# Kernel optimization log

Measured on AMD Instinct MI355X. Metric: run time of the kernel, lower is better.

## Reference

```python
import jax, jax.numpy as jnp
import numpy as np

H = 64          # hidden_size
NG = 5000       # num_genes
B = 32          # num_graphs
N = B * NG      # total nodes
E = 1_600_000   # total edges


def setup_inputs() -> dict:
    key = jax.random.key(0)
    ks = jax.random.split(key, 32)
    def nrm(k, shape, s=0.05):
        return jax.random.normal(k, shape, jnp.float32) * s
    return {
        "x": jax.random.normal(ks[0], (N, 2), jnp.float32),
        "edge_index": jax.random.randint(ks[1], (2, E), 0, N),
        # pert_w: Linear(1, H); gene_basal_w: Linear(1, H)
        "pert_w_W": nrm(ks[2], (H, 1)), "pert_w_b": nrm(ks[3], (H,)),
        "basal_W": nrm(ks[4], (H, 1)), "basal_b": nrm(ks[5], (H,)),
        # gene embedding table (max_norm=True -> rows renormed to norm<=1)
        "emb_table": nrm(ks[6], (NG, H), 0.5),
        # emb_trans: Linear(2H, H)
        "emb_trans_W": nrm(ks[7], (H, 2 * H)), "emb_trans_b": nrm(ks[8], (H,)),
        # pert_base_trans_w: Linear(2H, H)  (gene_pert_agg == 'concat+w')
        "pbt_W": nrm(ks[9], (H, 2 * H)), "pbt_b": nrm(ks[10], (H,)),
        # two GCNConv(H, H) layers
        "gcn1_W": nrm(ks[11], (H, H)), "gcn1_b": nrm(ks[12], (H,)),
        "gcn2_W": nrm(ks[13], (H, H)), "gcn2_b": nrm(ks[14], (H,)),
        # recovery_w: MLP([H, 2H, H, 1]) with BN on first two hidden layers
        "rec_W1": nrm(ks[15], (2 * H, H)), "rec_b1": nrm(ks[16], (2 * H,)),
        "rec_g1": jnp.ones((2 * H,), jnp.float32), "rec_be1": jnp.zeros((2 * H,), jnp.float32),
        "rec_W2": nrm(ks[17], (H, 2 * H)), "rec_b2": nrm(ks[18], (H,)),
        "rec_g2": jnp.ones((H,), jnp.float32), "rec_be2": jnp.zeros((H,), jnp.float32),
        "rec_W3": nrm(ks[19], (1, H)), "rec_b3": nrm(ks[20], (1,)),
    }


def _gcn_conv(h, src, dst, norm, W, b, n_nodes):
    # PyG GCNConv: x' = scatter_add(norm * (x W^T)[src] -> dst) + b, self-loops included in src/dst
    m = h @ W.T                                   # [N, H]
    out = jax.ops.segment_sum(m[src] * norm[:, None], dst, num_segments=n_nodes)
    return out + b


def _batchnorm(z, g, b, eps=1e-5):
    mu = z.mean(0)
    var = z.var(0)
    return (z - mu) * jax.lax.rsqrt(var + eps) * g + b


def reference(x, edge_index, pert_w_W, pert_w_b, basal_W, basal_b, emb_table,
              emb_trans_W, emb_trans_b, pbt_W, pbt_b, gcn1_W, gcn1_b,
              gcn2_W, gcn2_b, rec_W1, rec_b1, rec_g1, rec_be1,
              rec_W2, rec_b2, rec_g2, rec_be2, rec_W3, rec_b3):
    n_nodes = x.shape[0]
    ng = emb_table.shape[0]
    nb = n_nodes // ng

    # GCN normalization with self-loops (computed once, shared by both layers)
    loop = jnp.arange(n_nodes)
    src = jnp.concatenate([edge_index[0], loop])
    dst = jnp.concatenate([edge_index[1], loop])
    deg = jax.ops.segment_sum(jnp.ones_like(src, jnp.float32), dst, num_segments=n_nodes)
    dinv = jnp.where(deg > 0, jax.lax.rsqrt(jnp.maximum(deg, 1.0)), 0.0)
    norm = dinv[src] * dinv[dst]

    pert_emb = x[:, 1:2] @ pert_w_W.T + pert_w_b          # [N, H]
    base = x[:, 0:1] @ basal_W.T + basal_b                # [N, H]

    # nn.Embedding(max_norm=True): renorm rows to max L2 norm of 1
    nrm = jnp.linalg.norm(emb_table, axis=1, keepdims=True)
    emb_n = emb_table * jnp.minimum(1.0, 1.0 / jnp.maximum(nrm, 1e-7))
    emb = jnp.tile(emb_n, (nb, 1))                        # arange(NG).repeat(B) lookup
    base_emb = jnp.concatenate([emb, base], axis=1) @ emb_trans_W.T + emb_trans_b

    def pbt(p, b_):
        return jnp.concatenate([p, b_], axis=1) @ pbt_W.T + pbt_b

    h = pbt(pert_emb, base_emb)
    h = pbt(jax.nn.relu(_gcn_conv(h, src, dst, norm, gcn1_W, gcn1_b, n_nodes)), base_emb)
    h = pbt(jax.nn.relu(_gcn_conv(h, src, dst, norm, gcn2_W, gcn2_b, n_nodes)), base_emb)

    # recovery_w: Linear -> BN -> ReLU -> Linear -> BN -> ReLU -> Linear
    z = jax.nn.relu(_batchnorm(h @ rec_W1.T + rec_b1, rec_g1, rec_be1))
    z = jax.nn.relu(_batchnorm(z @ rec_W2.T + rec_b2, rec_g2, rec_be2))
    out = z @ rec_W3.T + rec_b3                           # [N, 1]
    return out.reshape(nb, ng)
```

## Files before the change

kernel.cpp:

```cpp
#include <hip/hip_runtime.h>


#define GS_GRID 2048
#define GS_BLK  256

enum { A1_=0, A0_=64, C1_=128, C0_=192, D1_=256, D0_=320,
       S1_=384, Q1_=512, SC1_=640, SH1_=768,
       S2_=896, Q2_=960, SC2_=1024, SH2_=1088,
       GD1_=1152, GA1_=1216, G00_=1280,
       GD2_=1344, G02_=1408, RD1_=1472, RD0_=1600, CST_FLOATS=2048 };

__device__ __forceinline__ float wave_sum64(float v) {
#pragma unroll
  for (int o = 32; o; o >>= 1) v += __shfl_xor(v, o, 64);
  return v;
}

__device__ __forceinline__ int rfl(int v) { return __builtin_amdgcn_readfirstlane(v); }

__device__ __forceinline__ float rlane(float v, int k) {
  return __int_as_float(__builtin_amdgcn_readlane(__float_as_int(v), k));
}


__global__ __launch_bounds__(256) void hist_k(const int* __restrict__ ei,
                                              int* __restrict__ hist, int E) {
  __shared__ int h[256];
  const int t = threadIdx.x;
  h[t] = 0;
  __syncthreads();
  const int per = (E + gridDim.x - 1) / gridDim.x;
  const int beg = blockIdx.x * per, end = min(E, beg + per);
  for (int i = beg + t; i < end; i += 256)
    atomicAdd(&h[ei[E + i] >> 10], 1);
  __syncthreads();
  hist[blockIdx.x * 256 + t] = h[t];
}

__global__ void scan1b_k(int* __restrict__ hist, int* __restrict__ bsum) {
  __shared__ int sc[256];
  const int t = threadIdx.x;
  const int b = blockIdx.x;
  int v = hist[t * 256 + b];
  sc[t] = v; __syncthreads();
  for (int o = 1; o < 256; o <<= 1) {
    int x = sc[t]; if (t >= o) x += sc[t - o];
    __syncthreads(); sc[t] = x; __syncthreads();
  }
  hist[t * 256 + b] = sc[t] - v;
  if (t == 255) bsum[b] = sc[t];
}

__global__ void scan2b_k(const int* __restrict__ bsum, int* __restrict__ bucketBase,
                         int* __restrict__ rowptrN, int E) {
  __shared__ int sc[256];
  const int t = threadIdx.x;
  int v = bsum[t];
  sc[t] = v; __syncthreads();
  for (int o = 1; o < 256; o <<= 1) {
    int x = sc[t]; if (t >= o) x += sc[t - o];
    __syncthreads(); sc[t] = x; __syncthreads();
  }
  bucketBase[t] = sc[t] - v;
  if (t == 255) { bucketBase[256] = sc[t]; rowptrN[0] = E; }
}

__global__ __launch_bounds__(256) void bucket_k(const int* __restrict__ ei,
                                                const int* __restrict__ hist,
                                                const int* __restrict__ bucketBase,
                                                int2* __restrict__ eb, int E) {
  __shared__ int cur[256];
  const int t = threadIdx.x;
  cur[t] = hist[blockIdx.x * 256 + t] + bucketBase[t];
  __syncthreads();
  const int per = (E + gridDim.x - 1) / gridDim.x;
  const int beg = blockIdx.x * per, end = min(E, beg + per);
// ... 69 lines not shown
  }
  cst[A1_ + h] = a1; cst[A0_ + h] = a0; cst[C1_ + h] = c1; cst[C0_ + h] = c0 + etB[h];
}

__global__ void consts2_k(const float* __restrict__ pbtW, const float* __restrict__ pbtB,
                          float* __restrict__ cst) {
  int h = threadIdx.x;
  float d1 = 0, d0 = 0;
  for (int k = 0; k < 64; ++k) {
    float w = pbtW[h * 128 + 64 + k];
    d1 = fmaf(w, cst[C1_ + k], d1);
    d0 = fmaf(w, cst[C0_ + k], d0);
  }
  cst[D1_ + h] = d1; cst[D0_ + h] = d0 + pbtB[h];
}

__global__ void consts3_k(const float* __restrict__ g1W, float* __restrict__ cst) {
  int h = threadIdx.x;
  float gd1 = 0, ga1 = 0, g00 = 0;
  for (int k = 0; k < 64; ++k) {
    float w = g1W[h * 64 + k];
    gd1 = fmaf(w, cst[D1_ + k], gd1);
    ga1 = fmaf(w, cst[A1_ + k], ga1);
    g00 = fmaf(w, cst[D0_ + k] + cst[A0_ + k], g00);
  }
  cst[GD1_ + h] = gd1; cst[GA1_ + h] = ga1; cst[G00_ + h] = g00;
}

__global__ void consts5_k(const float* __restrict__ g2W, float* __restrict__ cst) {
  int h = threadIdx.x;
  float a = 0, b = 0;
  for (int k = 0; k < 64; ++k) {
    float w = g2W[h * 64 + k];
    a = fmaf(w, cst[D1_ + k], a);
    b = fmaf(w, cst[D0_ + k], b);
  }
  cst[GD2_ + h] = a; cst[G02_ + h] = b;
}

__global__ void consts6_k(const float* __restrict__ rW1, const float* __restrict__ rb1,
                          float* __restrict__ cst) {
  int c = threadIdx.x;
  float a = 0, b = 0;
  for (int k = 0; k < 64; ++k) {
    float w = rW1[c * 64 + k];
    a = fmaf(w, cst[D1_ + k], a);
    b = fmaf(w, cst[D0_ + k], b);
  }
  cst[RD1_ + c] = a; cst[RD0_ + c] = b + rb1[c];
}

__global__ void constsW_k(const float* __restrict__ g2W, const float* __restrict__ rW1,
                          const float* __restrict__ pbtW,
                          float* __restrict__ Wf, float* __restrict__ Wr) {
  const int t = threadIdx.x;
  for (int e = t; e < 4096; e += 256) {
    int c = e >> 6, j = e & 63;
    float s = 0.f;
    for (int h = 0; h < 64; ++h) s = fmaf(g2W[c * 64 + h], pbtW[h * 128 + j], s);
    Wf[e] = s;
  }
  for (int e = t; e < 8192; e += 256) {
    int c = e >> 6, j = e & 63;
    float s = 0.f;
    for (int h = 0; h < 64; ++h) s = fmaf(rW1[c * 64 + h], pbtW[h * 128 + j], s);
    Wr[e] = s;
  }
}

template <bool NORM>
__global__ __launch_bounds__(256) void geneT_k(const float* __restrict__ in,
                                               const float* __restrict__ W, int ldw,
                                               float* __restrict__ out, int NG) {
  const int lane = threadIdx.x & 63;
  const int wid = blockIdx.x * 4 + (threadIdx.x >> 6);
  const int nw = gridDim.x * 4;
  float w[64];
#pragma unroll
  for (int j = 0; j < 16; ++j) {
    float4 v = *reinterpret_cast<const float4*>(W + lane * ldw + 4 * j);
    w[4 * j] = v.x; w[4 * j + 1] = v.y; w[4 * j + 2] = v.z; w[4 * j + 3] = v.w;
  }
  for (int g = wid; g < NG; g += nw) {
    float e = in[g * 64 + lane];
    if (NORM) {
      float sq = wave_sum64(e * e);
      float nrm = sqrtf(sq);
      float s = nrm > 1.f ? 1.f / nrm : 1.f;
      e *= s;
    }
    float acc = 0.f;
#pragma unroll
    for (int k = 0; k < 64; ++k) acc = fmaf(w[k], rlane(e, k), acc);
    out[g * 64 + lane] = acc;
  }
}

__global__ __launch_bounds__(256) void m1_k(const float* __restrict__ x,
                                            const float* __restrict__ embTm1,
                                            const float* __restrict__ dinv,
                                            const float* __restrict__ cst,
                                            float* __restrict__ m1, int N, int NG) {
  int total = N * 16;
  for (int idx = blockIdx.x * blockDim.x + threadIdx.x; idx < total;
       idx += gridDim.x * blockDim.x) {
    int n = idx >> 4, q = idx & 15;
    int g = n % NG;
    float x0 = x[2 * n], x1 = x[2 * n + 1], dn = dinv[n];
    float4 em = *reinterpret_cast<const float4*>(embTm1 + g * 64 + q * 4);
    float4 gd1 = *reinterpret_cast<const float4*>(cst + GD1_ + q * 4);
    float4 ga1 = *reinterpret_cast<const float4*>(cst + GA1_ + q * 4);
    float4 g00 = *reinterpret_cast<const float4*>(cst + G00_ + q * 4);
    float4 mv;
    mv.x = dn * (fmaf(x0, gd1.x, fmaf(x1, ga1.x, em.x + g00.x)));
    mv.y = dn * (fmaf(x0, gd1.y, fmaf(x1, ga1.y, em.y + g00.y)));
    mv.z = dn * (fmaf(x0, gd1.z, fmaf(x1, ga1.z, em.z + g00.z)));
    mv.w = dn * (fmaf(x0, gd1.w, fmaf(x1, ga1.w, em.w + g00.w)));
    reinterpret_cast<float4*>(m1)[idx] = mv;
  }
}

#define XS_STRIDE 130
#define WS_STRIDE 68
#define OS_STRIDE 68
#define OS_WORDS  (128 * OS_STRIDE)
#define WS_WORDS  (64 * WS_STRIDE)
#define LDS_WORDS (OS_WORDS + WS_WORDS + 128)

template <bool MUL_D>
__global__ __launch_bounds__(256, 4) void gemmt_gv_k(
    const float* __restrict__ in,
    const float* __restrict__ W,
    const float* __restrict__ tbl,
    const float* __restrict__ cA,
    const float* __restrict__ cB,
    const float* __restrict__ x,
    const float* __restrict__ dinv,
    float* __restrict__ out, int ldout, int N, int NG) {
  __shared__ float lds[LDS_WORDS];
  float* Xs = lds;
  float* Ws = lds + OS_WORDS;
  const int t = threadIdx.x;
  const int base = blockIdx.x << 7;

#pragma unroll
  for (int c = 0; c < 16; ++c) {
    int lin = c * 256 + t;
    int cw = lin >> 6, kw = lin & 63;
    Ws[kw * WS_STRIDE + cw] = W[cw * 64 + kw];
  }
#pragma unroll
  for (int c = 0; c < 8; ++c) {
    int lin = c * 256 + t;
    int nl = lin >> 4, k4 = lin & 15;
    int row = base + nl; if (row >= N) row = N - 1;
    float4 v = *reinterpret_cast<const float4*>(in + (size_t)row * 64 + 4 * k4);
    Xs[(4 * k4 + 0) * XS_STRIDE + nl] = v.x;
    Xs[(4 * k4 + 1) * XS_STRIDE + nl] = v.y;
    Xs[(4 * k4 + 2) * XS_STRIDE + nl] = v.z;
    Xs[(4 * k4 + 3) * XS_STRIDE + nl] = v.w;
  }
  __syncthreads();

  const int ng = t & 31;
  const int c0 = (t >> 5) * 8;
  float acc[8][4];
#pragma unroll
  for (int i = 0; i < 8; ++i)
#pragma unroll
    for (int j = 0; j < 4; ++j) acc[i][j] = 0.f;
#pragma unroll 4
  for (int k = 0; k < 64; ++k) {
    float4 wa = *reinterpret_cast<const float4*>(Ws + k * WS_STRIDE + c0);
    float4 wb = *reinterpret_cast<const float4*>(Ws + k * WS_STRIDE + c0 + 4);
    float2 xa = *reinterpret_cast<const float2*>(Xs + k * XS_STRIDE + 2 * ng);
    float2 xb = *reinterpret_cast<const float2*>(Xs + k * XS_STRIDE + 2 * ng + 64);
    const float w8[8] = {wa.x, wa.y, wa.z, wa.w, wb.x, wb.y, wb.z, wb.w};
    const float x4[4] = {xa.x, xa.y, xb.x, xb.y};
#pragma unroll
    for (int ci = 0; ci < 8; ++ci)
#pragma unroll
      for (int xi = 0; xi < 4; ++xi)
        acc[ci][xi] = fmaf(w8[ci], x4[xi], acc[ci][xi]);
  }
  __syncthreads();

  const int nd[4] = {2 * ng, 2 * ng + 1, 2 * ng + 64, 2 * ng + 65};
#pragma unroll
  for (int ci = 0; ci < 8; ++ci) {
    Xs[nd[0] * OS_STRIDE + c0 + ci] = acc[ci][0];
    Xs[nd[1] * OS_STRIDE + c0 + ci] = acc[ci][1];
    Xs[nd[2] * OS_STRIDE + c0 + ci] = acc[ci][2];
    Xs[nd[3] * OS_STRIDE + c0 + ci] = acc[ci][3];
  }
  __syncthreads();

  const int q = t & 15;
  const float4 a4 = *reinterpret_cast<const float4*>(cA + 4 * q);
  const float4 b4 = *reinterpret_cast<const float4*>(cB + 4 * q);
#pragma unroll
  for (int c = 0; c < 8; ++c) {
    int nl = c * 16 + (t >> 4);
    int n = base + nl;
    if (n < N) {
      float4 o = *reinterpret_cast<const float4*>(Xs + nl * OS_STRIDE + 4 * q);
      int g = n % NG;
      float4 tg = *reinterpret_cast<const float4*>(tbl + (size_t)g * 64 + 4 * q);
      float x0 = x[2 * n];
      o.x += fmaf(x0, a4.x, tg.x + b4.x);
      o.y += fmaf(x0, a4.y, tg.y + b4.y);
      o.z += fmaf(x0, a4.z, tg.z + b4.z);
      o.w += fmaf(x0, a4.w, tg.w + b4.w);
      if (MUL_D) {
        float dv = dinv[n];
        o.x *= dv; o.y *= dv; o.z *= dv; o.w *= dv;
      }
      *reinterpret_cast<float4*>(out + (size_t)n * ldout + 4 * q) = o;
    }
  }
}

__global__ __launch_bounds__(256, 4) void gemmt_rec1_k(
    const float* __restrict__ in,
    const float* __restrict__ Wr,
    const float* __restrict__ tblA, const float* __restrict__ tblB,
    const float* __restrict__ cA,
    const float* __restrict__ cB,
    const float* __restrict__ x,
    float* __restrict__ Z,
    float* __restrict__ sums, float* __restrict__ sqs,
    int N, int NG) {
  __shared__ float lds[LDS_WORDS];
  float* Xs = lds;
  float* Ws = lds + OS_WORDS;
  float* sred = lds + OS_WORDS + WS_WORDS;
  const int t = threadIdx.x;
  const int base = blockIdx.x << 7;
  if (t < 128) sred[t] = 0.f;

#pragma unroll
  for (int c = 0; c < 16; ++c) {
    int lin = c * 256 + t;
    int cw = lin >> 6, kw = lin & 63;
    Ws[kw * WS_STRIDE + cw] = Wr[cw * 64 + kw];
  }
#pragma unroll
  for (int c = 0; c < 8; ++c) {
    int lin = c * 256 + t;
    int nl = lin >> 4, k4 = lin & 15;
    int row = base + nl; if (row >= N) row = N - 1;
    float4 v = *reinterpret_cast<const float4*>(in + (size_t)row * 64 + 4 * k4);
    Xs[(4 * k4 + 0) * XS_STRIDE + nl] = v.x;
    Xs[(4 * k4 + 1) * XS_STRIDE + nl] = v.y;
    Xs[(4 * k4 + 2) * XS_STRIDE + nl] = v.z;
    Xs[(4 * k4 + 3) * XS_STRIDE + nl] = v.w;
  }
  __syncthreads();

  const int ng = t & 31;
  const int c0 = (t >> 5) * 8;
  float accA[8][4], accB[8][4];
#pragma unroll
  for (int i = 0; i < 8; ++i)
#pragma unroll
    for (int j = 0; j < 4; ++j) { accA[i][j] = 0.f; accB[i][j] = 0.f; }

#pragma unroll 4
  for (int k = 0; k < 64; ++k) {
    float4 wa = *reinterpret_cast<const float4*>(Ws + k * WS_STRIDE + c0);
    float4 wb = *reinterpret_cast<const float4*>(Ws + k * WS_STRIDE + c0 + 4);
    float2 xa = *reinterpret_cast<const float2*>(Xs + k * XS_STRIDE + 2 * ng);
    float2 xb = *reinterpret_cast<const float2*>(Xs + k * XS_STRIDE + 2 * ng + 64);
    const float w8[8] = {wa.x, wa.y, wa.z, wa.w, wb.x, wb.y, wb.z, wb.w};
    const float x4[4] = {xa.x, xa.y, xb.x, xb.y};
#pragma unroll
    for (int ci = 0; ci < 8; ++ci)
#pragma unroll
      for (int xi = 0; xi < 4; ++xi)
        accA[ci][xi] = fmaf(w8[ci], x4[xi], accA[ci][xi]);
  }
  __syncthreads();
#pragma unroll
  for (int c = 0; c < 16; ++c) {
    int lin = c * 256 + t;
    int cw = lin >> 6, kw = lin & 63;
    Ws[kw * WS_STRIDE + cw] = Wr[(64 + cw) * 64 + kw];
  }
  __syncthreads();
#pragma unroll 4
  for (int k = 0; k < 64; ++k) {
    float4 wa = *reinterpret_cast<const float4*>(Ws + k * WS_STRIDE + c0);
    float4 wb = *reinterpret_cast<const float4*>(Ws + k * WS_STRIDE + c0 + 4);
    float2 xa = *reinterpret_cast<const float2*>(Xs + k * XS_STRIDE + 2 * ng);
    float2 xb = *reinterpret_cast<const float2*>(Xs + k * XS_STRIDE + 2 * ng + 64);
    const float w8[8] = {wa.x, wa.y, wa.z, wa.w, wb.x, wb.y, wb.z, wb.w};
    const float x4[4] = {xa.x, xa.y, xb.x, xb.y};
#pragma unroll
    for (int ci = 0; ci < 8; ++ci)
#pragma unroll
      for (int xi = 0; xi < 4; ++xi)
        accB[ci][xi] = fmaf(w8[ci], x4[xi], accB[ci][xi]);
  }
  __syncthreads();

  const int nd[4] = {2 * ng, 2 * ng + 1, 2 * ng + 64, 2 * ng + 65};
  const int q = t & 15;

#pragma unroll
  for (int ci = 0; ci < 8; ++ci) {
    Xs[nd[0] * OS_STRIDE + c0 + ci] = accA[ci][0];
    Xs[nd[1] * OS_STRIDE + c0 + ci] = accA[ci][1];
    Xs[nd[2] * OS_STRIDE + c0 + ci] = accA[ci][2];
    Xs[nd[3] * OS_STRIDE + c0 + ci] = accA[ci][3];
  }
  __syncthreads();
  {
    const float4 a4 = *reinterpret_cast<const float4*>(cA + 4 * q);
    const float4 b4 = *reinterpret_cast<const float4*>(cB + 4 * q);
    float4 s4 = make_float4(0.f, 0.f, 0.f, 0.f);
    float4 q4 = make_float4(0.f, 0.f, 0.f, 0.f);
#pragma unroll
    for (int c = 0; c < 8; ++c) {
      int nl = c * 16 + (t >> 4);
      int n = base + nl;
      if (n < N) {
        float4 o = *reinterpret_cast<const float4*>(Xs + nl * OS_STRIDE + 4 * q);
        int g = n % NG;
        float4 tg = *reinterpret_cast<const float4*>(tblA + (size_t)g * 64 + 4 * q);
        float x0 = x[2 * n];
        o.x += fmaf(x0, a4.x, tg.x + b4.x);
        o.y += fmaf(x0, a4.y, tg.y + b4.y);
        o.z += fmaf(x0, a4.z, tg.z + b4.z);
        o.w += fmaf(x0, a4.w, tg.w + b4.w);
        *reinterpret_cast<float4*>(Z + (size_t)n * 128 + 4 * q) = o;
        s4.x += o.x; s4.y += o.y; s4.z += o.z; s4.w += o.w;
        q4.x += o.x * o.x; q4.y += o.y * o.y; q4.z += o.z * o.z; q4.w += o.w * o.w;
      }
    }
    atomicAdd(&sred[4 * q + 0], s4.x); atomicAdd(&sred[4 * q + 1], s4.y);
    atomicAdd(&sred[4 * q + 2], s4.z); atomicAdd(&sred[4 * q + 3], s4.w);
    atomicAdd(&sred[64 + 4 * q + 0], q4.x); atomicAdd(&sred[64 + 4 * q + 1], q4.y);
    atomicAdd(&sred[64 + 4 * q + 2], q4.z); atomicAdd(&sred[64 + 4 * q + 3], q4.w);
  }
  __syncthreads();
  if (t < 64) {
    atomicAdd(&sums[t], sred[t]);
    atomicAdd(&sqs[t], sred[64 + t]);
  }
  __syncthreads();
  if (t < 128) sred[t] = 0.f;
  __syncthreads();

#pragma unroll
  for (int ci = 0; ci < 8; ++ci) {
    Xs[nd[0] * OS_STRIDE + c0 + ci] = accB[ci][0];
    Xs[nd[1] * OS_STRIDE + c0 + ci] = accB[ci][1];
    Xs[nd[2] * OS_STRIDE + c0 + ci] = accB[ci][2];
    Xs[nd[3] * OS_STRIDE + c0 + ci] = accB[ci][3];
  }
  __syncthreads();
  {
    const float4 a4 = *reinterpret_cast<const float4*>(cA + 64 + 4 * q);
    const float4 b4 = *reinterpret_cast<const float4*>(cB + 64 + 4 * q);
    float4 s4 = make_float4(0.f, 0.f, 0.f, 0.f);
    float4 q4 = make_float4(0.f, 0.f, 0.f, 0.f);
#pragma unroll
    for (int c = 0; c < 8; ++c) {
      int nl = c * 16 + (t >> 4);
      int n = base + nl;
      if (n < N) {
        float4 o = *reinterpret_cast<const float4*>(Xs + nl * OS_STRIDE + 4 * q);
        int g = n % NG;
        float4 tg = *reinterpret_cast<const float4*>(tblB + (size_t)g * 64 + 4 * q);
        float x0 = x[2 * n];
        o.x += fmaf(x0, a4.x, tg.x + b4.x);
        o.y += fmaf(x0, a4.y, tg.y + b4.y);
        o.z += fmaf(x0, a4.z, tg.z + b4.z);
        o.w += fmaf(x0, a4.w, tg.w + b4.w);
        *reinterpret_cast<float4*>(Z + (size_t)n * 128 + 64 + 4 * q) = o;
        s4.x += o.x; s4.y += o.y; s4.z += o.z; s4.w += o.w;
        q4.x += o.x * o.x; q4.y += o.y * o.y; q4.z += o.z * o.z; q4.w += o.w * o.w;
      }
    }
    atomicAdd(&sred[4 * q + 0], s4.x); atomicAdd(&sred[4 * q + 1], s4.y);
    atomicAdd(&sred[4 * q + 2], s4.z); atomicAdd(&sred[4 * q + 3], s4.w);
    atomicAdd(&sred[64 + 4 * q + 0], q4.x); atomicAdd(&sred[64 + 4 * q + 1], q4.y);
    atomicAdd(&sred[64 + 4 * q + 2], q4.z); atomicAdd(&sred[64 + 4 * q + 3], q4.w);
  }
  __syncthreads();
  if (t < 64) {
    atomicAdd(&sums[64 + t], sred[t]);
    atomicAdd(&sqs[64 + t], sred[64 + t]);
  }
}

__global__ __launch_bounds__(256, 4) void gemmt_rec2_k(
    const float* __restrict__ Z,
    const float* __restrict__ W,
    const float* __restrict__ b,
    const float* __restrict__ bnsc, const float* __restrict__ bnsh,
    float* __restrict__ out,
    float* __restrict__ sums, float* __restrict__ sqs, int N) {
  __shared__ float lds[LDS_WORDS];
  float* Xs = lds;
  float* Ws = lds + OS_WORDS;
  float* sred = lds + OS_WORDS + WS_WORDS;
  const int t = threadIdx.x;
  const int base = blockIdx.x << 7;
  if (t < 128) sred[t] = 0.f;

  const int ng = t & 31;
  const int c0 = (t >> 5) * 8;
  float acc[8][4];
#pragma unroll
  for (int i = 0; i < 8; ++i)
#pragma unroll
    for (int j = 0; j < 4; ++j) acc[i][j] = 0.f;

  for (int half = 0; half < 2; ++half) {
    if (half) __syncthreads();
    const int ko = half * 64;
#pragma unroll
    for (int c = 0; c < 16; ++c) {
      int lin = c * 256 + t;
      int cw = lin >> 6, kw = lin & 63;
      Ws[kw * WS_STRIDE + cw] = W[cw * 128 + ko + kw];
    }
#pragma unroll
    for (int c = 0; c < 8; ++c) {
      int lin = c * 256 + t;
      int nl = lin >> 4, k4 = lin & 15;
      int row = base + nl; if (row >= N) row = N - 1;
      float4 v = *reinterpret_cast<const float4*>(Z + (size_t)row * 128 + ko + 4 * k4);
      float4 sc = *reinterpret_cast<const float4*>(bnsc + ko + 4 * k4);
      float4 sh = *reinterpret_cast<const float4*>(bnsh + ko + 4 * k4);
      v.x = fmaxf(fmaf(v.x, sc.x, sh.x), 0.f);
      v.y = fmaxf(fmaf(v.y, sc.y, sh.y), 0.f);
      v.z = fmaxf(fmaf(v.z, sc.z, sh.z), 0.f);
      v.w = fmaxf(fmaf(v.w, sc.w, sh.w), 0.f);
      Xs[(4 * k4 + 0) * XS_STRIDE + nl] = v.x;
      Xs[(4 * k4 + 1) * XS_STRIDE + nl] = v.y;
      Xs[(4 * k4 + 2) * XS_STRIDE + nl] = v.z;
      Xs[(4 * k4 + 3) * XS_STRIDE + nl] = v.w;
    }
    __syncthreads();
#pragma unroll 4
    for (int k = 0; k < 64; ++k) {
      float4 wa = *reinterpret_cast<const float4*>(Ws + k * WS_STRIDE + c0);
      float4 wb = *reinterpret_cast<const float4*>(Ws + k * WS_STRIDE + c0 + 4);
      float2 xa = *reinterpret_cast<const float2*>(Xs + k * XS_STRIDE + 2 * ng);
      float2 xb = *reinterpret_cast<const float2*>(Xs + k * XS_STRIDE + 2 * ng + 64);
      const float w8[8] = {wa.x, wa.y, wa.z, wa.w, wb.x, wb.y, wb.z, wb.w};
      const float x4[4] = {xa.x, xa.y, xb.x, xb.y};
#pragma unroll
      for (int ci = 0; ci < 8; ++ci)
#pragma unroll
        for (int xi = 0; xi < 4; ++xi)
          acc[ci][xi] = fmaf(w8[ci], x4[xi], acc[ci][xi]);
    }
  }
  __syncthreads();

  const int nd[4] = {2 * ng, 2 * ng + 1, 2 * ng + 64, 2 * ng + 65};
#pragma unroll
  for (int ci = 0; ci < 8; ++ci) {
    Xs[nd[0] * OS_STRIDE + c0 + ci] = acc[ci][0];
    Xs[nd[1] * OS_STRIDE + c0 + ci] = acc[ci][1];
    Xs[nd[2] * OS_STRIDE + c0 + ci] = acc[ci][2];
    Xs[nd[3] * OS_STRIDE + c0 + ci] = acc[ci][3];
  }
  __syncthreads();

  const int q = t & 15;
  const float4 bb = *reinterpret_cast<const float4*>(b + 4 * q);
  float4 s4 = make_float4(0.f, 0.f, 0.f, 0.f);
  float4 q4 = make_float4(0.f, 0.f, 0.f, 0.f);
#pragma unroll
  for (int c = 0; c < 8; ++c) {
    int nl = c * 16 + (t >> 4);
    int n = base + nl;
    if (n < N) {
      float4 o = *reinterpret_cast<const float4*>(Xs + nl * OS_STRIDE + 4 * q);
      o.x += bb.x; o.y += bb.y; o.z += bb.z; o.w += bb.w;
      *reinterpret_cast<float4*>(out + (size_t)n * 64 + 4 * q) = o;
      s4.x += o.x; s4.y += o.y; s4.z += o.z; s4.w += o.w;
      q4.x += o.x * o.x; q4.y += o.y * o.y; q4.z += o.z * o.z; q4.w += o.w * o.w;
    }
  }
  atomicAdd(&sred[4 * q + 0], s4.x); atomicAdd(&sred[4 * q + 1], s4.y);
  atomicAdd(&sred[4 * q + 2], s4.z); atomicAdd(&sred[4 * q + 3], s4.w);
  atomicAdd(&sred[64 + 4 * q + 0], q4.x); atomicAdd(&sred[64 + 4 * q + 1], q4.y);
  atomicAdd(&sred[64 + 4 * q + 2], q4.z); atomicAdd(&sred[64 + 4 * q + 3], q4.w);
  __syncthreads();
  if (t < 64) {
    atomicAdd(&sums[t], sred[t]);
    atomicAdd(&sqs[t], sred[64 + t]);
  }
}

__global__ __launch_bounds__(256) void gather_k(const float* __restrict__ m,
                                                const int* __restrict__ rowptr,
                                                const int* __restrict__ col,
                                                const float* __restrict__ dinv,
                                                const float* __restrict__ bias,
                                                float* __restrict__ out, int N) {
  const int lane = threadIdx.x & 63;
  const int wid = blockIdx.x * 4 + (threadIdx.x >> 6);
  const int nw = gridDim.x * 4;
  const float b = bias[lane];
  for (int n = wid; n < N; n += nw) {
    const int nn = rfl(n);
    const float dn = dinv[nn];
    float a0 = m[(size_t)nn * 64 + lane];
    float a1 = 0.f, a2 = 0.f, a3 = 0.f;
    const int beg = rfl(rowptr[nn]), end = rfl(rowptr[nn + 1]);
    for (int base = beg; base < end; base += 64) {
      const int rem = end - base;
      const int kk = rem < 64 ? rem : 64;
      int cv = (lane < kk) ? col[base + lane] : 0;
      int k = 0;
      for (; k + 7 < kk; k += 8) {
        int i0 = __shfl(cv, k, 64),     i1 = __shfl(cv, k + 1, 64);
        int i2 = __shfl(cv, k + 2, 64), i3 = __shfl(cv, k + 3, 64);
        int i4 = __shfl(cv, k + 4, 64), i5 = __shfl(cv, k + 5, 64);
        int i6 = __shfl(cv, k + 6, 64), i7 = __shfl(cv, k + 7, 64);
        float v0 = m[(size_t)i0 * 64 + lane];
        float v1 = m[(size_t)i1 * 64 + lane];
        float v2 = m[(size_t)i2 * 64 + lane];
        float v3 = m[(size_t)i3 * 64 + lane];
        float v4 = m[(size_t)i4 * 64 + lane];
        float v5 = m[(size_t)i5 * 64 + lane];
        float v6 = m[(size_t)i6 * 64 + lane];
        float v7 = m[(size_t)i7 * 64 + lane];
        a0 += v0 + v4; a1 += v1 + v5; a2 += v2 + v6; a3 += v3 + v7;
      }
// ... 36 lines not shown
  const float sc = scale[lane], sh = shift[lane], w = W3[lane], b = b3[0];
  for (int n = wid; n < N; n += nw) {
    float v = z2[(size_t)n * 64 + lane];
    v = fmaxf(fmaf(v, sc, sh), 0.f) * w;
    v = wave_sum64(v);
    if (lane == 0) out[n] = v + b;
  }
}

extern "C" void kernel_launch(void* const* d_in, const int* in_sizes, int n_in,
                              void* d_out, int out_size, void* d_ws, size_t ws_size,
                              hipStream_t stream) {
  const float* x     = (const float*)d_in[0];
  const int*   ei    = (const int*)d_in[1];
  const float* pertW = (const float*)d_in[2];
  const float* pertB = (const float*)d_in[3];
  const float* basW  = (const float*)d_in[4];
  const float* basB  = (const float*)d_in[5];
  const float* embTb = (const float*)d_in[6];
  const float* etW   = (const float*)d_in[7];
  const float* etB   = (const float*)d_in[8];
  const float* pbtW  = (const float*)d_in[9];
  const float* pbtB  = (const float*)d_in[10];
  const float* g1W   = (const float*)d_in[11];
  const float* g1B   = (const float*)d_in[12];
  const float* g2W   = (const float*)d_in[13];
  const float* g2B   = (const float*)d_in[14];
  const float* rW1   = (const float*)d_in[15];
  const float* rb1   = (const float*)d_in[16];
  const float* rg1   = (const float*)d_in[17];
  const float* rbe1  = (const float*)d_in[18];
  const float* rW2   = (const float*)d_in[19];
  const float* rb2   = (const float*)d_in[20];
  const float* rg2   = (const float*)d_in[21];
  const float* rbe2  = (const float*)d_in[22];
  const float* rW3   = (const float*)d_in[23];
  const float* rb3   = (const float*)d_in[24];
  float* outp = (float*)d_out;

  const int N  = in_sizes[0] / 2;
  const int E  = in_sizes[1] / 2;
  const int NG = in_sizes[6] / 64;
  const int NB = (N + 1023) >> 10;
  const int NT = (N + 127) >> 7;

  char* p = (char*)d_ws;
  float* cst    = (float*)p; p += CST_FLOATS * 4;
  int*   hist   = (int*)p;   p += 256 * 256 * 4;
  int*   bb     = (int*)p;   p += 1024;
  int*   bsum   = (int*)p;   p += 1024;
  int*   rowptr = (int*)p;   p += (size_t)(N + 64) * 4;
  float* dinv   = (float*)p; p += (size_t)N * 4;
  int*   col    = (int*)p;   p += (size_t)E * 4;
  float* Wf     = (float*)p; p += 4096 * 4;
  float* Wr     = (float*)p; p += 8192 * 4;
  float* embT   = (float*)p; p += (size_t)NG * 64 * 4;
  float* embT2  = (float*)p; p += (size_t)NG * 64 * 4;
  float* embT2g2= (float*)p; p += (size_t)NG * 64 * 4;
  float* embT2rA= (float*)p; p += (size_t)NG * 64 * 4;
  float* embT2rB= (float*)p; p += (size_t)NG * 64 * 4;
  float* z2buf  = (float*)p; p += (size_t)N * 64 * 4;
  float* hb     = (float*)p; p += (size_t)N * 64 * 4;
  float* tmp1   = (float*)p; p += (size_t)N * 64 * 4;
  float* tmp2   = (float*)p; p += (size_t)N * 64 * 4;
  float* Z = hb;
  float* z2 = z2buf;
  float* embTm1 = embT;
  int2*  eb = (int2*)tmp2;

  dim3 blk(GS_BLK), grid(GS_GRID);

  hipMemsetAsync(cst, 0, CST_FLOATS * 4, stream);

  hist_k<<<256, 256, 0, stream>>>(ei, hist, E);
  scan1b_k<<<256, 256, 0, stream>>>(hist, bsum);
  scan2b_k<<<1, 256, 0, stream>>>(bsum, bb, rowptr + N, E);
  bucket_k<<<256, 256, 0, stream>>>(ei, hist, bb, eb, E);
  csr_k<<<NB, 256, 0, stream>>>(eb, bb, rowptr, dinv, col, N);

  consts1_k<<<1, 64, 0, stream>>>(pbtW, pertW, pertB, etW, basW, basB, etB, cst);
  consts2_k<<<1, 64, 0, stream>>>(pbtW, pbtB, cst);
  consts3_k<<<1, 64, 0, stream>>>(g1W, cst);
  consts5_k<<<1, 64, 0, stream>>>(g2W, cst);
  consts6_k<<<1, 128, 0, stream>>>(rW1, rb1, cst);
  constsW_k<<<1, 256, 0, stream>>>(g2W, rW1, pbtW, Wf, Wr);
  geneT_k<true><<<256, 256, 0, stream>>>(embTb, etW, 128, embT, NG);
  geneT_k<false><<<256, 256, 0, stream>>>(embT, pbtW + 64, 128, embT2, NG);
  geneT_k<false><<<256, 256, 0, stream>>>(embT2, g1W, 64, embTm1, NG);
  geneT_k<false><<<256, 256, 0, stream>>>(embT2, g2W, 64, embT2g2, NG);
  geneT_k<false><<<256, 256, 0, stream>>>(embT2, rW1, 64, embT2rA, NG);
  geneT_k<false><<<256, 256, 0, stream>>>(embT2, rW1 + 64 * 64, 64, embT2rB, NG);
  m1_k<<<grid, blk, 0, stream>>>(x, embTm1, dinv, cst, tmp1, N, NG);

  gather_k<<<grid, blk, 0, stream>>>(tmp1, rowptr, col, dinv, g1B, tmp2, N);
  gemmt_gv_k<true><<<NT, blk, 0, stream>>>(
      tmp2, Wf, embT2g2, cst + GD2_, cst + G02_, x, dinv, tmp1, 64, N, NG);
  gather_k<<<grid, blk, 0, stream>>>(tmp1, rowptr, col, dinv, g2B, tmp2, N);

  gemmt_rec1_k<<<NT, blk, 0, stream>>>(
      tmp2, Wr, embT2rA, embT2rB, cst + RD1_, cst + RD0_, x, Z,
      cst + S1_, cst + Q1_, N, NG);
  bnparam_k<<<1, 128, 0, stream>>>(cst + S1_, cst + Q1_, rg1, rbe1,
                                   cst + SC1_, cst + SH1_, 128, 1.0f / (float)N);
  gemmt_rec2_k<<<NT, blk, 0, stream>>>(Z, rW2, rb2, cst + SC1_, cst + SH1_,
                                       z2, cst + S2_, cst + Q2_, N);
  bnparam_k<<<1, 64, 0, stream>>>(cst + S2_, cst + Q2_, rg2, rbe2,
                                  cst + SC2_, cst + SH2_, 64, 1.0f / (float)N);
  rec3_k<<<grid, blk, 0, stream>>>(z2, cst + SC2_, cst + SH2_, rW3, rb3, outp, N);
}
```

Baseline: 485.9 us.

## Read pre-transposed GEMM weights wave-uniformly from global instead of LDS staging

The three node-wise GEMM kernels stop staging weight tiles in shared memory. They read pre-transposed weights (built once by constsW_k and a new w2t_k) directly from global memory with wave-uniform addresses, so each wave owns a slice of output columns. Thread mapping changes to 2 nodes by 16 or 32 columns per lane, and rec1 now computes all 128 outputs in one pass instead of two. This removes LDS weight traffic and some barriers, at the cost of more accumulator registers and more global/scalar weight loads per k step.

```diff
diff --git a/kernel.cpp b/kernel.cpp
--- a/kernel.cpp
+++ b/kernel.cpp
@@ -21,7 +21,6 @@
 __device__ __forceinline__ float rlane(float v, int k) {
   return __int_as_float(__builtin_amdgcn_readlane(__float_as_int(v), k));
 }
-
 
 __global__ __launch_bounds__(256) void hist_k(const int* __restrict__ ei,
                                               int* __restrict__ hist, int E) {
@@ -197,19 +196,26 @@
 
 __global__ void constsW_k(const float* __restrict__ g2W, const float* __restrict__ rW1,
                           const float* __restrict__ pbtW,
-                          float* __restrict__ Wf, float* __restrict__ Wr) {
+                          float* __restrict__ WfT, float* __restrict__ WrT) {
   const int t = threadIdx.x;
   for (int e = t; e < 4096; e += 256) {
     int c = e >> 6, j = e & 63;
     float s = 0.f;
     for (int h = 0; h < 64; ++h) s = fmaf(g2W[c * 64 + h], pbtW[h * 128 + j], s);
-    Wf[e] = s;
+    WfT[j * 64 + c] = s;
   }
   for (int e = t; e < 8192; e += 256) {
     int c = e >> 6, j = e & 63;
     float s = 0.f;
     for (int h = 0; h < 64; ++h) s = fmaf(rW1[c * 64 + h], pbtW[h * 128 + j], s);
-    Wr[e] = s;
+    WrT[j * 128 + c] = s;
+  }
+}
+
+__global__ void w2t_k(const float* __restrict__ rW2, float* __restrict__ W2T) {
+  for (int e = threadIdx.x; e < 8192; e += 256) {
+    int k = e >> 6, c = e & 63;
+    W2T[k * 64 + c] = rW2[c * 128 + k];
   }
 }
 
@@ -266,77 +272,66 @@
 }
 
 #define XS_STRIDE 130
-#define WS_STRIDE 68
-#define OS_STRIDE 68
-#define OS_WORDS  (128 * OS_STRIDE)
-#define WS_WORDS  (64 * WS_STRIDE)
-#define LDS_WORDS (OS_WORDS + WS_WORDS + 128)
-
-template <bool MUL_D>
-__global__ __launch_bounds__(256, 4) void gemmt_gv_k(
-    const float* __restrict__ in,
-    const float* __restrict__ W,
-    const float* __restrict__ tbl,
-    const float* __restrict__ cA,
-    const float* __restrict__ cB,
-    const float* __restrict__ x,
-    const float* __restrict__ dinv,
-    float* __restrict__ out, int ldout, int N, int NG) {
-  __shared__ float lds[LDS_WORDS];
-  float* Xs = lds;
-  float* Ws = lds + OS_WORDS;
-  const int t = threadIdx.x;
-  const int base = blockIdx.x << 7;
-
-#pragma unroll
-  for (int c = 0; c < 16; ++c) {
-    int lin = c * 256 + t;
-    int cw = lin >> 6, kw = lin & 63;
-    Ws[kw * WS_STRIDE + cw] = W[cw * 64 + kw];
-  }
+#define OS_STRIDE 65
+#define LDS_WORDS (64 * XS_STRIDE + 128)
+
+__device__ __forceinline__ void stage_x64(const float* __restrict__ in, int ldin,
+                                          int inOff, int base, int N, float* Xs, int t) {
 #pragma unroll
   for (int c = 0; c < 8; ++c) {
     int lin = c * 256 + t;
     int nl = lin >> 4, k4 = lin & 15;
     int row = base + nl; if (row >= N) row = N - 1;
-    float4 v = *reinterpret_cast<const float4*>(in + (size_t)row * 64 + 4 * k4);
+    float4 v = *reinterpret_cast<const float4*>(in + (size_t)row * ldin + inOff + 4 * k4);
     Xs[(4 * k4 + 0) * XS_STRIDE + nl] = v.x;
     Xs[(4 * k4 + 1) * XS_STRIDE + nl] = v.y;
     Xs[(4 * k4 + 2) * XS_STRIDE + nl] = v.z;
     Xs[(4 * k4 + 3) * XS_STRIDE + nl] = v.w;
   }
-  __syncthreads();
-
-  const int ng = t & 31;
-  const int c0 = (t >> 5) * 8;
-  float acc[8][4];
-#pragma unroll
-  for (int i = 0; i < 8; ++i)
-#pragma unroll
-    for (int j = 0; j < 4; ++j) acc[i][j] = 0.f;
+}
+
+template <bool MUL_D>
+__global__ __launch_bounds__(256, 4) void gemmt_gv_k(
+    const float* __restrict__ in,
+    const float* __restrict__ WT,
+    const float* __restrict__ tbl,
+    const float* __restrict__ cA, const float* __restrict__ cB,
+    const float* __restrict__ x, const float* __restrict__ dinv,
+    float* __restrict__ out, int ldout, int N, int NG) {
+  __shared__ float Xs[LDS_WORDS];
+  const int t = threadIdx.x;
+  const int base = blockIdx.x << 7;
+  stage_x64(in, 64, 0, base, N, Xs, t);
+  __syncthreads();
+
+  const int w = rfl(t >> 6);
+  const int lane = t & 63;
+  const int n0 = 2 * lane;
+  float acc[16][2];
+#pragma unroll
+  for (int i = 0; i < 16; ++i) { acc[i][0] = 0.f; acc[i][1] = 0.f; }
+  const float* __restrict__ wt = WT + 16 * w;
 #pragma unroll 4
   for (int k = 0; k < 64; ++k) {
-    float4 wa = *reinterpret_cast<const float4*>(Ws + k * WS_STRIDE + c0);
-    float4 wb = *reinterpret_cast<const float4*>(Ws + k * WS_STRIDE + c0 + 4);
-    float2 xa = *reinterpret_cast<const float2*>(Xs + k * XS_STRIDE + 2 * ng);
-    float2 xb = *reinterpret_cast<const float2*>(Xs + k * XS_STRIDE + 2 * ng + 64);
-    const float w8[8] = {wa.x, wa.y, wa.z, wa.w, wb.x, wb.y, wb.z, wb.w};
-    const float x4[4] = {xa.x, xa.y, xb.x, xb.y};
-#pragma unroll
-    for (int ci = 0; ci < 8; ++ci)
-#pragma unroll
-      for (int xi = 0; xi < 4; ++xi)
-        acc[ci][xi] = fmaf(w8[ci], x4[xi], acc[ci][xi]);
-  }
-  __syncthreads();
-
-  const int nd[4] = {2 * ng, 2 * ng + 1, 2 * ng + 64, 2 * ng + 65};
-#pragma unroll
-  for (int ci = 0; ci < 8; ++ci) {
-    Xs[nd[0] * OS_STRIDE + c0 + ci] = acc[ci][0];
-    Xs[nd[1] * OS_STRIDE + c0 + ci] = acc[ci][1];
-    Xs[nd[2] * OS_STRIDE + c0 + ci] = acc[ci][2];
-    Xs[nd[3] * OS_STRIDE + c0 + ci] = acc[ci][3];
+    const float* wr = wt + k * 64;
+    float4 w0 = *reinterpret_cast<const float4*>(wr);
+    float4 w1 = *reinterpret_cast<const float4*>(wr + 4);
+    float4 w2 = *reinterpret_cast<const float4*>(wr + 8);
+    float4 w3 = *reinterpret_cast<const float4*>(wr + 12);
+    float2 xv = *reinterpret_cast<const float2*>(Xs + k * XS_STRIDE + n0);
+    const float wv[16] = {w0.x, w0.y, w0.z, w0.w, w1.x, w1.y, w1.z, w1.w,
+                          w2.x, w2.y, w2.z, w2.w, w3.x, w3.y, w3.z, w3.w};
+#pragma unroll
+    for (int ci = 0; ci < 16; ++ci) {
+      acc[ci][0] = fmaf(wv[ci], xv.x, acc[ci][0]);
+      acc[ci][1] = fmaf(wv[ci], xv.y, acc[ci][1]);
+    }
+  }
+  __syncthreads();
+#pragma unroll
+  for (int ci = 0; ci < 16; ++ci) {
+    Xs[n0 * OS_STRIDE + 16 * w + ci] = acc[ci][0];
+    Xs[(n0 + 1) * OS_STRIDE + 16 * w + ci] = acc[ci][1];
   }
   __syncthreads();
 
@@ -348,7 +343,8 @@
     int nl = c * 16 + (t >> 4);
     int n = base + nl;
     if (n < N) {
-      float4 o = *reinterpret_cast<const float4*>(Xs + nl * OS_STRIDE + 4 * q);
+      const float* os = Xs + nl * OS_STRIDE + 4 * q;
+      float4 o = make_float4(os[0], os[1], os[2], os[3]);
       int g = n % NG;
       float4 tg = *reinterpret_cast<const float4*>(tbl + (size_t)g * 64 + 4 * q);
       float x0 = x[2 * n];
@@ -367,101 +363,63 @@
 
 __global__ __launch_bounds__(256, 4) void gemmt_rec1_k(
     const float* __restrict__ in,
-    const float* __restrict__ Wr,
+    const float* __restrict__ WrT,
     const float* __restrict__ tblA, const float* __restrict__ tblB,
-    const float* __restrict__ cA,
-    const float* __restrict__ cB,
+    const float* __restrict__ cA, const float* __restrict__ cB,
     const float* __restrict__ x,
     float* __restrict__ Z,
-    float* __restrict__ sums, float* __restrict__ sqs,
-    int N, int NG) {
-  __shared__ float lds[LDS_WORDS];
-  float* Xs = lds;
-  float* Ws = lds + OS_WORDS;
-  float* sred = lds + OS_WORDS + WS_WORDS;
+    float* __restrict__ sums, float* __restrict__ sqs, int N, int NG) {
+  __shared__ float Xs[LDS_WORDS];
+  float* sred = Xs + 64 * XS_STRIDE;
   const int t = threadIdx.x;
   const int base = blockIdx.x << 7;
-  if (t < 128) sred[t] = 0.f;
-
-#pragma unroll
-  for (int c = 0; c < 16; ++c) {
-    int lin = c * 256 + t;
-    int cw = lin >> 6, kw = lin & 63;
-    Ws[kw * WS_STRIDE + cw] = Wr[cw * 64 + kw];
-  }
-#pragma unroll
-  for (int c = 0; c < 8; ++c) {
-    int lin = c * 256 + t;
-    int nl = lin >> 4, k4 = lin & 15;
-    int row = base + nl; if (row >= N) row = N - 1;
-    float4 v = *reinterpret_cast<const float4*>(in + (size_t)row * 64 + 4 * k4);
-    Xs[(4 * k4 + 0) * XS_STRIDE + nl] = v.x;
-    Xs[(4 * k4 + 1) * XS_STRIDE + nl] = v.y;
-    Xs[(4 * k4 + 2) * XS_STRIDE + nl] = v.z;
-    Xs[(4 * k4 + 3) * XS_STRIDE + nl] = v.w;
-  }
-  __syncthreads();
-
-  const int ng = t & 31;
-  const int c0 = (t >> 5) * 8;
-  float accA[8][4], accB[8][4];
-#pragma unroll
-  for (int i = 0; i < 8; ++i)
-#pragma unroll
-    for (int j = 0; j < 4; ++j) { accA[i][j] = 0.f; accB[i][j] = 0.f; }
-
-#pragma unroll 4
+  stage_x64(in, 64, 0, base, N, Xs, t);
+  __syncthreads();
+
+  const int w = rfl(t >> 6);
+  const int lane = t & 63;
+  const int n0 = 2 * lane;
+  float acc[32][2];
+#pragma unroll
+  for (int i = 0; i < 32; ++i) { acc[i][0] = 0.f; acc[i][1] = 0.f; }
+  const float* __restrict__ wt = WrT + 32 * w;
+#pragma unroll 2
   for (int k = 0; k < 64; ++k) {
-    float4 wa = *reinterpret_cast<const float4*>(Ws + k * WS_STRIDE + c0);
-    float4 wb = *reinterpret_cast<const float4*>(Ws + k * WS_STRIDE + c0 + 4);
-    float2 xa = *reinterpret_cast<const float2*>(Xs + k * XS_STRIDE + 2 * ng);
-    float2 xb = *reinterpret_cast<const float2*>(Xs + k * XS_STRIDE + 2 * ng + 64);
-    const float w8[8] = {wa.x, wa.y, wa.z, wa.w, wb.x, wb.y, wb.z, wb.w};
-    const float x4[4] = {xa.x, xa.y, xb.x, xb.y};
-#pragma unroll
-    for (int ci = 0; ci < 8; ++ci)
-#pragma unroll
-      for (int xi = 0; xi < 4; ++xi)
-        accA[ci][xi] = fmaf(w8[ci], x4[xi], accA[ci][xi]);
-  }
-  __syncthreads();
-#pragma unroll
-  for (int c = 0; c < 16; ++c) {
-    int lin = c * 256 + t;
-    int cw = lin >> 6, kw = lin & 63;
-    Ws[kw * WS_STRIDE + cw] = Wr[(64 + cw) * 64 + kw];
-  }
-  __syncthreads();
-#pragma unroll 4
-  for (int k = 0; k < 64; ++k) {
-    float4 wa = *reinterpret_cast<const float4*>(Ws + k * WS_STRIDE + c0);
-    float4 wb = *reinterpret_cast<const float4*>(Ws + k * WS_STRIDE + c0 + 4);
-    float2 xa = *reinterpret_cast<const float2*>(Xs + k * XS_STRIDE + 2 * ng);
-    float2 xb = *reinterpret_cast<const float2*>(Xs + k * XS_STRIDE + 2 * ng + 64);
-    const float w8[8] = {wa.x, wa.y, wa.z, wa.w, wb.x, wb.y, wb.z, wb.w};
-    const float x4[4] = {xa.x, xa.y, xb.x, xb.y};
-#pragma unroll
-    for (int ci = 0; ci < 8; ++ci)
-#pragma unroll
-      for (int xi = 0; xi < 4; ++xi)
-        accB[ci][xi] = fmaf(w8[ci], x4[xi], accB[ci][xi]);
-  }
-  __syncthreads();
-
-  const int nd[4] = {2 * ng, 2 * ng + 1, 2 * ng + 64, 2 * ng + 65};
+    const float* wr = wt + k * 128;
+    float4 wv4[8];
+#pragma unroll
+    for (int j = 0; j < 8; ++j) wv4[j] = *reinterpret_cast<const float4*>(wr + 4 * j);
+    float2 xv = *reinterpret_cast<const float2*>(Xs + k * XS_STRIDE + n0);
+#pragma unroll
+    for (int j = 0; j < 8; ++j) {
+      acc[4 * j + 0][0] = fmaf(wv4[j].x, xv.x, acc[4 * j + 0][0]);
+      acc[4 * j + 0][1] = fmaf(wv4[j].x, xv.y, acc[4 * j + 0][1]);
+      acc[4 * j + 1][0] = fmaf(wv4[j].y, xv.x, acc[4 * j + 1][0]);
+      acc[4 * j + 1][1] = fmaf(wv4[j].y, xv.y, acc[4 * j + 1][1]);
+      acc[4 * j + 2][0] = fmaf(wv4[j].z, xv.x, acc[4 * j + 2][0]);
+      acc[4 * j + 2][1] = fmaf(wv4[j].z, xv.y, acc[4 * j + 2][1]);
+      acc[4 * j + 3][0] = fmaf(wv4[j].w, xv.x, acc[4 * j + 3][0]);
+      acc[4 * j + 3][1] = fmaf(wv4[j].w, xv.y, acc[4 * j + 3][1]);
+    }
+  }
+  __syncthreads();
+
   const int q = t & 15;
-
-#pragma unroll
-  for (int ci = 0; ci < 8; ++ci) {
-    Xs[nd[0] * OS_STRIDE + c0 + ci] = accA[ci][0];
-    Xs[nd[1] * OS_STRIDE + c0 + ci] = accA[ci][1];
-    Xs[nd[2] * OS_STRIDE + c0 + ci] = accA[ci][2];
-    Xs[nd[3] * OS_STRIDE + c0 + ci] = accA[ci][3];
-  }
-  __syncthreads();
-  {
-    const float4 a4 = *reinterpret_cast<const float4*>(cA + 4 * q);
-    const float4 b4 = *reinterpret_cast<const float4*>(cB + 4 * q);
+  for (int r = 0; r < 2; ++r) {
+    if (r) __syncthreads();
+    if ((w >> 1) == r) {
+      const int cb = 32 * (w & 1);
+#pragma unroll
+      for (int ci = 0; ci < 32; ++ci) {
+        Xs[n0 * OS_STRIDE + cb + ci] = acc[ci][0];
+        Xs[(n0 + 1) * OS_STRIDE + cb + ci] = acc[ci][1];
+      }
+    }
+    if (t < 128) sred[t] = 0.f;
+    __syncthreads();
+    const float* tbl = r ? tblB : tblA;
+    const float4 a4 = *reinterpret_cast<const float4*>(cA + 64 * r + 4 * q);
+    const float4 b4 = *reinterpret_cast<const float4*>(cB + 64 * r + 4 * q);
     float4 s4 = make_float4(0.f, 0.f, 0.f, 0.f);
     float4 q4 = make_float4(0.f, 0.f, 0.f, 0.f);
 #pragma unroll
@@ -469,15 +427,16 @@
       int nl = c * 16 + (t >> 4);
       int n = base + nl;
       if (n < N) {
-        float4 o = *reinterpret_cast<const float4*>(Xs + nl * OS_STRIDE + 4 * q);
+        const float* os = Xs + nl * OS_STRIDE + 4 * q;
+        float4 o = make_float4(os[0], os[1], os[2], os[3]);
         int g = n % NG;
-        float4 tg = *reinterpret_cast<const float4*>(tblA + (size_t)g * 64 + 4 * q);
+        float4 tg = *reinterpret_cast<const float4*>(tbl + (size_t)g * 64 + 4 * q);
         float x0 = x[2 * n];
         o.x += fmaf(x0, a4.x, tg.x + b4.x);
         o.y += fmaf(x0, a4.y, tg.y + b4.y);
         o.z += fmaf(x0, a4.z, tg.z + b4.z);
         o.w += fmaf(x0, a4.w, tg.w + b4.w);
-        *reinterpret_cast<float4*>(Z + (size_t)n * 128 + 4 * q) = o;
+        *reinterpret_cast<float4*>(Z + (size_t)n * 128 + 64 * r + 4 * q) = o;
         s4.x += o.x; s4.y += o.y; s4.z += o.z; s4.w += o.w;
         q4.x += o.x * o.x; q4.y += o.y * o.y; q4.z += o.z * o.z; q4.w += o.w * o.w;
       }
@@ -486,91 +445,37 @@
     atomicAdd(&sred[4 * q + 2], s4.z); atomicAdd(&sred[4 * q + 3], s4.w);
     atomicAdd(&sred[64 + 4 * q + 0], q4.x); atomicAdd(&sred[64 + 4 * q + 1], q4.y);
     atomicAdd(&sred[64 + 4 * q + 2], q4.z); atomicAdd(&sred[64 + 4 * q + 3], q4.w);
-  }
-  __syncthreads();
-  if (t < 64) {
-    atomicAdd(&sums[t], sred[t]);
-    atomicAdd(&sqs[t], sred[64 + t]);
-  }
-  __syncthreads();
-  if (t < 128) sred[t] = 0.f;
-  __syncthreads();
-
-#pragma unroll
-  for (int ci = 0; ci < 8; ++ci) {
-    Xs[nd[0] * OS_STRIDE + c0 + ci] = accB[ci][0];
-    Xs[nd[1] * OS_STRIDE + c0 + ci] = accB[ci][1];
-    Xs[nd[2] * OS_STRIDE + c0 + ci] = accB[ci][2];
-    Xs[nd[3] * OS_STRIDE + c0 + ci] = accB[ci][3];
-  }
-  __syncthreads();
-  {
-    const float4 a4 = *reinterpret_cast<const float4*>(cA + 64 + 4 * q);
-    const float4 b4 = *reinterpret_cast<const float4*>(cB + 64 + 4 * q);
-    float4 s4 = make_float4(0.f, 0.f, 0.f, 0.f);
-    float4 q4 = make_float4(0.f, 0.f, 0.f, 0.f);
-#pragma unroll
-    for (int c = 0; c < 8; ++c) {
-      int nl = c * 16 + (t >> 4);
-      int n = base + nl;
-      if (n < N) {
-        float4 o = *reinterpret_cast<const float4*>(Xs + nl * OS_STRIDE + 4 * q);
-        int g = n % NG;
-        float4 tg = *reinterpret_cast<const float4*>(tblB + (size_t)g * 64 + 4 * q);
-        float x0 = x[2 * n];
-        o.x += fmaf(x0, a4.x, tg.x + b4.x);
-        o.y += fmaf(x0, a4.y, tg.y + b4.y);
-        o.z += fmaf(x0, a4.z, tg.z + b4.z);
-        o.w += fmaf(x0, a4.w, tg.w + b4.w);
-        *reinterpret_cast<float4*>(Z + (size_t)n * 128 + 64 + 4 * q) = o;
-        s4.x += o.x; s4.y += o.y; s4.z += o.z; s4.w += o.w;
-        q4.x += o.x * o.x; q4.y += o.y * o.y; q4.z += o.z * o.z; q4.w += o.w * o.w;
-      }
-    }
-    atomicAdd(&sred[4 * q + 0], s4.x); atomicAdd(&sred[4 * q + 1], s4.y);
-    atomicAdd(&sred[4 * q + 2], s4.z); atomicAdd(&sred[4 * q + 3], s4.w);
-    atomicAdd(&sred[64 + 4 * q + 0], q4.x); atomicAdd(&sred[64 + 4 * q + 1], q4.y);
-    atomicAdd(&sred[64 + 4 * q + 2], q4.z); atomicAdd(&sred[64 + 4 * q + 3], q4.w);
-  }
-  __syncthreads();
-  if (t < 64) {
-    atomicAdd(&sums[64 + t], sred[t]);
-    atomicAdd(&sqs[64 + t], sred[64 + t]);
+    __syncthreads();
+    if (t < 64) {
+      atomicAdd(&sums[64 * r + t], sred[t]);
+      atomicAdd(&sqs[64 * r + t], sred[64 + t]);
+    }
   }
 }
 
 __global__ __launch_bounds__(256, 4) void gemmt_rec2_k(
     const float* __restrict__ Z,
-    const float* __restrict__ W,
+    const float* __restrict__ W2T,
     const float* __restrict__ b,
     const float* __restrict__ bnsc, const float* __restrict__ bnsh,
     float* __restrict__ out,
     float* __restrict__ sums, float* __restrict__ sqs, int N) {
-  __shared__ float lds[LDS_WORDS];
-  float* Xs = lds;
-  float* Ws = lds + OS_WORDS;
-  float* sred = lds + OS_WORDS + WS_WORDS;
+  __shared__ float Xs[LDS_WORDS];
+  float* sred = Xs + 64 * XS_STRIDE;
   const int t = threadIdx.x;
   const int base = blockIdx.x << 7;
   if (t < 128) sred[t] = 0.f;
 
-  const int ng = t & 31;
-  const int c0 = (t >> 5) * 8;
-  float acc[8][4];
-#pragma unroll
-  for (int i = 0; i < 8; ++i)
-#pragma unroll
-    for (int j = 0; j < 4; ++j) acc[i][j] = 0.f;
+  const int w = rfl(t >> 6);
+  const int lane = t & 63;
+  const int n0 = 2 * lane;
+  float acc[16][2];
+#pragma unroll
+  for (int i = 0; i < 16; ++i) { acc[i][0] = 0.f; acc[i][1] = 0.f; }
 
   for (int half = 0; half < 2; ++half) {
     if (half) __syncthreads();
     const int ko = half * 64;
-#pragma unroll
-    for (int c = 0; c < 16; ++c) {
-      int lin = c * 256 + t;
-      int cw = lin >> 6, kw = lin & 63;
-      Ws[kw * WS_STRIDE + cw] = W[cw * 128 + ko + kw];
-    }
 #pragma unroll
     for (int c = 0; c < 8; ++c) {
       int lin = c * 256 + t;
@@ -589,30 +494,29 @@
       Xs[(4 * k4 + 3) * XS_STRIDE + nl] = v.w;
     }
     __syncthreads();
+    const float* __restrict__ wt = W2T + (size_t)ko * 64 + 16 * w;
 #pragma unroll 4
     for (int k = 0; k < 64; ++k) {
-      float4 wa = *reinterpret_cast<const float4*>(Ws + k * WS_STRIDE + c0);
-      float4 wb = *reinterpret_cast<const float4*>(Ws + k * WS_STRIDE + c0 + 4);
-      float2 xa = *reinterpret_cast<const float2*>(Xs + k * XS_STRIDE + 2 * ng);
-      float2 xb = *reinterpret_cast<const float2*>(Xs + k * XS_STRIDE + 2 * ng + 64);
-      const float w8[8] = {wa.x, wa.y, wa.z, wa.w, wb.x, wb.y, wb.z, wb.w};
-      const float x4[4] = {xa.x, xa.y, xb.x, xb.y};
-#pragma unroll
-      for (int ci = 0; ci < 8; ++ci)
-#pragma unroll
-        for (int xi = 0; xi < 4; ++xi)
-          acc[ci][xi] = fmaf(w8[ci], x4[xi], acc[ci][xi]);
-    }
-  }
-  __syncthreads();
-
-  const int nd[4] = {2 * ng, 2 * ng + 1, 2 * ng + 64, 2 * ng + 65};
-#pragma unroll
-  for (int ci = 0; ci < 8; ++ci) {
-    Xs[nd[0] * OS_STRIDE + c0 + ci] = acc[ci][0];
-    Xs[nd[1] * OS_STRIDE + c0 + ci] = acc[ci][1];
-    Xs[nd[2] * OS_STRIDE + c0 + ci] = acc[ci][2];
-    Xs[nd[3] * OS_STRIDE + c0 + ci] = acc[ci][3];
+      const float* wr = wt + k * 64;
+      float4 w0 = *reinterpret_cast<const float4*>(wr);
+      float4 w1 = *reinterpret_cast<const float4*>(wr + 4);
+      float4 w2 = *reinterpret_cast<const float4*>(wr + 8);
+      float4 w3 = *reinterpret_cast<const float4*>(wr + 12);
+      float2 xv = *reinterpret_cast<const float2*>(Xs + k * XS_STRIDE + n0);
+      const float wv[16] = {w0.x, w0.y, w0.z, w0.w, w1.x, w1.y, w1.z, w1.w,
+                            w2.x, w2.y, w2.z, w2.w, w3.x, w3.y, w3.z, w3.w};
+#pragma unroll
+      for (int ci = 0; ci < 16; ++ci) {
+        acc[ci][0] = fmaf(wv[ci], xv.x, acc[ci][0]);
+        acc[ci][1] = fmaf(wv[ci], xv.y, acc[ci][1]);
+      }
+    }
+  }
+  __syncthreads();
+#pragma unroll
+  for (int ci = 0; ci < 16; ++ci) {
+    Xs[n0 * OS_STRIDE + 16 * w + ci] = acc[ci][0];
+    Xs[(n0 + 1) * OS_STRIDE + 16 * w + ci] = acc[ci][1];
   }
   __syncthreads();
 
@@ -625,7 +529,8 @@
     int nl = c * 16 + (t >> 4);
     int n = base + nl;
     if (n < N) {
-      float4 o = *reinterpret_cast<const float4*>(Xs + nl * OS_STRIDE + 4 * q);
+      const float* os = Xs + nl * OS_STRIDE + 4 * q;
+      float4 o = make_float4(os[0], os[1], os[2], os[3]);
       o.x += bb.x; o.y += bb.y; o.z += bb.z; o.w += bb.w;
       *reinterpret_cast<float4*>(out + (size_t)n * 64 + 4 * q) = o;
       s4.x += o.x; s4.y += o.y; s4.z += o.z; s4.w += o.w;
@@ -768,8 +673,9 @@
   int*   rowptr = (int*)p;   p += (size_t)(N + 64) * 4;
   float* dinv   = (float*)p; p += (size_t)N * 4;
   int*   col    = (int*)p;   p += (size_t)E * 4;
-  float* Wf     = (float*)p; p += 4096 * 4;
-  float* Wr     = (float*)p; p += 8192 * 4;
+  float* WfT    = (float*)p; p += 4096 * 4;
+  float* WrT    = (float*)p; p += 8192 * 4;
+  float* W2T    = (float*)p; p += 8192 * 4;
   float* embT   = (float*)p; p += (size_t)NG * 64 * 4;
   float* embT2  = (float*)p; p += (size_t)NG * 64 * 4;
   float* embT2g2= (float*)p; p += (size_t)NG * 64 * 4;
@@ -799,7 +705,8 @@
   consts3_k<<<1, 64, 0, stream>>>(g1W, cst);
   consts5_k<<<1, 64, 0, stream>>>(g2W, cst);
   consts6_k<<<1, 128, 0, stream>>>(rW1, rb1, cst);
-  constsW_k<<<1, 256, 0, stream>>>(g2W, rW1, pbtW, Wf, Wr);
+  constsW_k<<<1, 256, 0, stream>>>(g2W, rW1, pbtW, WfT, WrT);
+  w2t_k<<<1, 256, 0, stream>>>(rW2, W2T);
   geneT_k<true><<<256, 256, 0, stream>>>(embTb, etW, 128, embT, NG);
   geneT_k<false><<<256, 256, 0, stream>>>(embT, pbtW + 64, 128, embT2, NG);
   geneT_k<false><<<256, 256, 0, stream>>>(embT2, g1W, 64, embTm1, NG);
@@ -810,15 +717,15 @@
 
   gather_k<<<grid, blk, 0, stream>>>(tmp1, rowptr, col, dinv, g1B, tmp2, N);
   gemmt_gv_k<true><<<NT, blk, 0, stream>>>(
-      tmp2, Wf, embT2g2, cst + GD2_, cst + G02_, x, dinv, tmp1, 64, N, NG);
+      tmp2, WfT, embT2g2, cst + GD2_, cst + G02_, x, dinv, tmp1, 64, N, NG);
   gather_k<<<grid, blk, 0, stream>>>(tmp1, rowptr, col, dinv, g2B, tmp2, N);
 
   gemmt_rec1_k<<<NT, blk, 0, stream>>>(
-      tmp2, Wr, embT2rA, embT2rB, cst + RD1_, cst + RD0_, x, Z,
+      tmp2, WrT, embT2rA, embT2rB, cst + RD1_, cst + RD0_, x, Z,
       cst + S1_, cst + Q1_, N, NG);
   bnparam_k<<<1, 128, 0, stream>>>(cst + S1_, cst + Q1_, rg1, rbe1,
                                    cst + SC1_, cst + SH1_, 128, 1.0f / (float)N);
-  gemmt_rec2_k<<<NT, blk, 0, stream>>>(Z, rW2, rb2, cst + SC1_, cst + SH1_,
+  gemmt_rec2_k<<<NT, blk, 0, stream>>>(Z, W2T, rb2, cst + SC1_, cst + SH1_,
                                        z2, cst + S2_, cst + Q2_, N);
   bnparam_k<<<1, 64, 0, stream>>>(cst + S2_, cst + Q2_, rg2, rbe2,
                                   cst + SC2_, cst + SH2_, 64, 1.0f / (float)N);
```

After: 526.7 us. 1.08x slower.
